# Kernel tuning notes

Measured on AMD Instinct MI355X. Metric: run time of the kernel, lower is better.

The kernel has to match this reference:

```python
import jax, jax.numpy as jnp
import numpy as np

N = 50000      # total packed nodes
E = 1600000    # edges (no self loops; layers add them)
G = 64         # graphs in the batch
F_IN = 24      # raw node feature dim
D = 64         # hidden dim
H = 4          # attention heads
C = D // H     # 16 channels per head
L = 3          # GAT layers
NEG = 0.2      # LeakyReLU negative slope (GATv2 default)
EPS = 1e-5     # LayerNorm eps


def setup_inputs() -> dict:
    key = jax.random.key(0)
    ks = jax.random.split(key, 16)
    x = jax.random.normal(ks[0], (N, F_IN), jnp.float32)
    src = jax.random.randint(ks[1], (E,), 0, N)
    dst = jax.random.randint(ks[2], (E,), 0, N)
    dst = jnp.where(dst == src, (dst + 1) % N, dst)  # keep edge list self-loop free
    edge_index = jnp.stack([src, dst]).astype(jnp.int32)
    batch = jnp.sort(jax.random.randint(ks[3], (N,), 0, G)).astype(jnp.int32)
    s = 0.1
    return dict(
        x=x, edge_index=edge_index, batch=batch,
        w_in=jax.random.normal(ks[4], (F_IN, D), jnp.float32) * s,
        b_in=jnp.zeros((D,), jnp.float32),
        w_l=jax.random.normal(ks[5], (L, D, D), jnp.float32) * s,
        b_l=jnp.zeros((L, D), jnp.float32),
        w_r=jax.random.normal(ks[6], (L, D, D), jnp.float32) * s,
        b_r=jnp.zeros((L, D), jnp.float32),
        att=jax.random.normal(ks[7], (L, H, C), jnp.float32) * s,
        b_gat=jnp.zeros((L, D), jnp.float32),
        ln_g=jnp.ones((L, D), jnp.float32),
        ln_b=jnp.zeros((L, D), jnp.float32),
        w_g1=jax.random.normal(ks[8], (D, D // 2), jnp.float32) * s,
        b_g1=jnp.zeros((D // 2,), jnp.float32),
        w_g2=jax.random.normal(ks[9], (D // 2, 1), jnp.float32) * s,
        b_g2=jnp.zeros((1,), jnp.float32),
        w_out=jax.random.normal(ks[10], (D, D), jnp.float32) * s,
        b_out=jnp.zeros((D,), jnp.float32),
    )


def _layernorm(h, g, b):
    m = h.mean(-1, keepdims=True)
    v = ((h - m) ** 2).mean(-1, keepdims=True)
    return (h - m) * jax.lax.rsqrt(v + EPS) * g + b


def _gatv2(h, src, dst, wl, bl, wr, br, att, bg):
    n = h.shape[0]
    xl = (h @ wl + bl).reshape(n, H, C)   # source transform
    xr = (h @ wr + br).reshape(n, H, C)   # target transform
    # edge scores: att . leaky_relu(xl[j] + xr[i])  -> [E', H]
    e = jnp.sum(jax.nn.leaky_relu(xl[src] + xr[dst], NEG) * att, axis=-1)
    emax = jax.ops.segment_max(e, dst, num_segments=n)
    ex = jnp.exp(e - emax[dst])
    denom = jax.ops.segment_sum(ex, dst, num_segments=n)
    alpha = ex / denom[dst]               # segment softmax over incoming edges
    out = jax.ops.segment_sum(alpha[:, :, None] * xl[src], dst, num_segments=n)
    return out.reshape(n, D) + bg


def reference(x, edge_index, batch, w_in, b_in, w_l, b_l, w_r, b_r, att, b_gat,
              ln_g, ln_b, w_g1, b_g1, w_g2, b_g2, w_out, b_out):
    n = x.shape[0]
    loops = jnp.arange(n, dtype=edge_index.dtype)
    src = jnp.concatenate([edge_index[0], loops])  # add self loops once
    dst = jnp.concatenate([edge_index[1], loops])
    h = jax.nn.relu(x @ w_in + b_in)
    for i in range(L):
        res = h
        h = _gatv2(h, src, dst, w_l[i], b_l[i], w_r[i], b_r[i], att[i], b_gat[i])
        h = _layernorm(h + res, ln_g[i], ln_b[i])
        if i < L - 1:
            h = jax.nn.relu(h)
    # GlobalAttention pooling: gate MLP -> per-graph softmax -> weighted sum
    gate = jax.nn.relu(h @ w_g1 + b_g1) @ w_g2 + b_g2  # [N, 1]
    gmax = jax.ops.segment_max(gate, batch, num_segments=G)
    ge = jnp.exp(gate - gmax[batch])
    gs = jax.ops.segment_sum(ge, batch, num_segments=G)
    a = ge / jnp.where(gs > 0, gs, 1.0)[batch]
    emb = jax.ops.segment_sum(a * h, batch, num_segments=G)  # [G, D]
    return jax.nn.relu(emb @ w_out + b_out)
```

## Files before the change

kernel.cpp:

```cpp
#include <hip/hip_runtime.h>

#define NEGS   0.2f
#define LN_EPS 1e-5f
#define BSH    7
#define BN     128
#define TILE   4096
#define LOG2E  1.44269504f

typedef const float* __restrict__ fp;
typedef _Float16 v2h __attribute__((ext_vector_type(2)));
typedef _Float16 v8h __attribute__((ext_vector_type(8)));
typedef float    v4f __attribute__((ext_vector_type(4)));

__device__ __forceinline__ v2h u2h(unsigned u){ union{unsigned u; v2h h;} c; c.u = u; return c.h; }
__device__ __forceinline__ unsigned h2u(v2h h){ union{v2h h; unsigned u;} c; c.h = h; return c.u; }

template<int CTRL>
__device__ __forceinline__ float dppadd(float x){
  int y = __builtin_amdgcn_update_dpp(0, __float_as_int(x), CTRL, 0xF, 0xF, true);
  return x + __int_as_float(y);
}
__device__ __forceinline__ float hsum8(float s){
  s = dppadd<0xB1>(s);
  s = dppadd<0x4E>(s);
  s = dppadd<0x141>(s);
  return s;
}

__device__ __forceinline__ float dot8(v8h a, v8h b, float init){
  union U { v8h v; v2h h[4]; };
  U ua; ua.v = a;
  U ub; ub.v = b;
  float s = init;
  #pragma unroll
  for (int i = 0; i < 4; ++i) s = __builtin_amdgcn_fdot2(ua.h[i], ub.h[i], s, false);
  return s;
}

__device__ __forceinline__ v8h leaky8(v8h t){
  return __builtin_elementwise_max(t, t * (_Float16)NEGS);
}

__device__ __forceinline__ float edge_w8(v8h v, v8h xr8, v8h att8, float negm2){
  v8h t = leaky8(v + xr8);
  float s = dppadd<0xB1>(dot8(t, att8, negm2));
  return __builtin_amdgcn_exp2f(s);
}

__global__ __launch_bounds__(256) void k_setup(fp x, fp w, fp b, float* __restrict__ h,
                                               unsigned* __restrict__ h16, int N,
                                               fp w_l, fp w_r, fp att,
                                               _Float16* __restrict__ wf, _Float16* __restrict__ att16,
                                               float* __restrict__ gz, int nz,
                                               const int* __restrict__ dstA, int* __restrict__ counts,
                                               int E, int K, int ntiles){
  __shared__ float ws[24*64];
  __shared__ float bs[64];
  __shared__ float xs[4][24];
  __shared__ int hist[512];
  int tid = threadIdx.x;
  if (blockIdx.x < 6){
    int lm = blockIdx.x;
    if (lm < 3){
      for (int d = tid; d < 64; d += 256)
        att16[lm*64 + d] = (_Float16)(att[lm*64 + d] * LOG2E);
    }
    for (int i = lm*256 + tid; i < nz; i += 6*256) gz[i] = 0.f;
    const float* src = ((lm & 1) ? w_r : w_l) + (lm >> 1)*4096;
    _Float16* dst = wf + lm*4096;
    for (int d = tid; d < 4096; d += 256){
      int jj = d & 7, l = (d >> 3) & 63, kc = (d >> 9) & 1, nt = d >> 10;
      int k = kc*32 + (l >> 4)*8 + jj;
      int n = nt*16 + (l & 15);
      dst[d] = (_Float16)src[k*64 + n];
    }
    return;
  }
  if (blockIdx.x < (unsigned)(6 + ntiles)){
    int t = blockIdx.x - 6;
    for (int i = tid; i < K; i += 256) hist[i] = 0;
    __syncthreads();
    int e0 = t*TILE, e1 = min(e0 + TILE, E);
    for (int e = e0 + tid; e < e1; e += 256)
      atomicAdd(&hist[dstA[e] >> BSH], 1);
    __syncthreads();
    for (int i = tid; i < K; i += 256) counts[i*ntiles + t] = hist[i];
    return;
  }
  int blk = blockIdx.x - 6 - ntiles;
  for (int i = tid; i < 24*64; i += 256) ws[i] = w[i];
  if (tid < 64) bs[tid] = b[tid];
  int r = tid >> 6, c = tid & 63;
  int row = blk*4 + r;
  if (c < 24 && row < N) xs[r][c] = x[row*24 + c];
  __syncthreads();
  float acc = bs[c];
  #pragma unroll
  for (int k = 0; k < 24; ++k) acc = fmaf(xs[r][k], ws[k*64 + c], acc);
  float y = fmaxf(acc, 0.f);
  float y1 = __shfl_down(y, 1);
  if (row < N){
    h[(size_t)row*64 + c] = y;
    if (!(c & 1)){
      v2h p; p.x = (_Float16)y; p.y = (_Float16)y1;
      h16[(size_t)row*32 + (c >> 1)] = h2u(p);
    }
  }
}

__global__ __launch_bounds__(512) void s_scan_tiles(int* __restrict__ counts, int* __restrict__ btotal,
                                                    int ntiles){
  __shared__ int s[512];
  int b = blockIdx.x, tid = threadIdx.x;
  int v = (tid < ntiles) ? counts[b*ntiles + tid] : 0;
  s[tid] = v;
  __syncthreads();
  for (int off = 1; off < 512; off <<= 1){
    int t = (tid >= off) ? s[tid - off] : 0;
    __syncthreads();
    s[tid] += t;
    __syncthreads();
  }
  if (tid < ntiles) counts[b*ntiles + tid] = s[tid] - v;
  if (tid == 511) btotal[b] = s[511];
}

__global__ __launch_bounds__(512) void s_scan_buckets(const int* __restrict__ btotal,
                                                      int* __restrict__ bbase, int K, int E){
  __shared__ int s[512];
  int tid = threadIdx.x;
  int v = (tid < K) ? btotal[tid] : 0;
  s[tid] = v;
  __syncthreads();
  for (int off = 1; off < 512; off <<= 1){
    int t = (tid >= off) ? s[tid - off] : 0;
    __syncthreads();
    s[tid] += t;
    __syncthreads();
  }
  if (tid < K) bbase[tid] = s[tid] - v;
  if (tid == 0) bbase[K] = E;
}

__global__ __launch_bounds__(256) void t_scatter(const int* __restrict__ srcA, const int* __restrict__ dstA,
                                                 const int* __restrict__ counts, const int* __restrict__ bbase,
                                                 unsigned* __restrict__ packed, int E, int K, int ntiles){
  __shared__ int gb[512];
  __shared__ int cur[512];
  int t = blockIdx.x, tid = threadIdx.x;
  for (int i = tid; i < K; i += 256){
    gb[i] = bbase[i] + counts[i*ntiles + t];
    cur[i] = 0;
  }
  __syncthreads();
  int e0 = t*TILE, e1 = min(e0 + TILE, E);
  for (int e = e0 + tid; e < e1; e += 256){
    int d = dstA[e], sv = srcA[e];
    int b = d >> BSH;
    int p = atomicAdd(&cur[b], 1);
    packed[gb[b] + p] = ((unsigned)(d & (BN-1)) << 25) | (unsigned)sv;
  }
}

__global__ __launch_bounds__(256) void k_finexfm(const unsigned* __restrict__ packed, const int* __restrict__ bbase,
                                                 int* __restrict__ row_ptr, int* __restrict__ col, int N, int K,
                                                 const unsigned* __restrict__ h16, const _Float16* __restrict__ wf,
                                                 fp blg, fp brg,
                                                 unsigned* __restrict__ xl16, unsigned* __restrict__ xr16){
  __shared__ int hist[BN];
  __shared__ int excl[BN];
  int tid = threadIdx.x;
  if (blockIdx.x < (unsigned)K){
    int b = blockIdx.x;
    int node0 = b << BSH;
    int e_base = bbase[b], e_end = bbase[b+1];
    if (tid < BN) hist[tid] = 0;
    __syncthreads();
    for (int e = e_base + tid; e < e_end; e += 256)
      atomicAdd(&hist[packed[e] >> 25], 1);
    __syncthreads();
    int v = (tid < BN) ? hist[tid] : 0;
    if (tid < BN) excl[tid] = v;
    __syncthreads();
    for (int off = 1; off < BN; off <<= 1){
      int t2 = 0;
      if (tid < BN && tid >= off) t2 = excl[tid - off];
      __syncthreads();
      if (tid < BN) excl[tid] += t2;
      __syncthreads();
    }
    int nn = min(BN, N - node0);
    if (tid < nn) row_ptr[node0 + tid] = e_base + excl[tid] - v;
    if (b == K-1 && tid == 0) row_ptr[N] = e_end;
    if (tid < BN) hist[tid] = excl[tid] - v;
    __syncthreads();
    for (int e = e_base + tid; e < e_end; e += 256){
      unsigned u = packed[e];
      int dl = u >> 25;
      int p = atomicAdd(&hist[dl], 1);
      col[e_base + p] = (int)(u & 0x1FFFFFFu);
    }
    return;
  }
  int xb = blockIdx.x - K;
  int wave = tid >> 6, lane = tid & 63;
  int quad = lane >> 4, ln = lane & 15;
  int m0 = xb*64 + wave*16;
  if (m0 >= N) return;
  int m = m0 + ln;
  bool mv = m < N;
  v8h a0 = {}, a1 = {};
  if (mv){
    a0 = *(const v8h*)&h16[(size_t)m*32 + quad*4];
    a1 = *(const v8h*)&h16[(size_t)m*32 + 16 + quad*4];
  }
  #pragma unroll
  for (int mat = 0; mat < 2; ++mat){
    const _Float16* wb = wf + mat*4096;
    fp bias = mat ? brg : blg;
    unsigned* dst = mat ? xr16 : xl16;
    #pragma unroll
    for (int nt = 0; nt < 4; ++nt){
      v8h b0 = *(const v8h*)&wb[nt*1024 + lane*8];
      v8h b1 = *(const v8h*)&wb[nt*1024 + 512 + lane*8];
      float bv = bias[nt*16 + ln];
      v4f acc = {bv, bv, bv, bv};
      acc = __builtin_amdgcn_mfma_f32_16x16x32_f16(a0, b0, acc, 0, 0, 0);
      acc = __builtin_amdgcn_mfma_f32_16x16x32_f16(a1, b1, acc, 0, 0, 0);
      #pragma unroll
      for (int r = 0; r < 4; ++r){
        float partner = __shfl_xor(acc[r], 1);
        int node = m0 + quad*4 + r;
        if (!(lane & 1) && node < N){
          v2h p; p.x = (_Float16)acc[r]; p.y = (_Float16)partner;
          dst[(size_t)node*32 + nt*8 + (ln >> 1)] = h2u(p);
        }
      }
    }
  }
}

__global__ __launch_bounds__(256) void k_xfm(const unsigned* __restrict__ h16,
                                             const _Float16* __restrict__ wf,
                                             fp blg, fp brg,
                                             unsigned* __restrict__ xl16, unsigned* __restrict__ xr16, int N){
  int tid = threadIdx.x, wave = tid >> 6, lane = tid & 63;
  int quad = lane >> 4, ln = lane & 15;
  int m0 = blockIdx.x*64 + wave*16;
  if (m0 >= N) return;
  int m = m0 + ln;
  bool mv = m < N;
  v8h a0 = {}, a1 = {};
  if (mv){
    a0 = *(const v8h*)&h16[(size_t)m*32 + quad*4];
    a1 = *(const v8h*)&h16[(size_t)m*32 + 16 + quad*4];
  }
  #pragma unroll
  for (int mat = 0; mat < 2; ++mat){
    const _Float16* wb = wf + mat*4096;
    fp bias = mat ? brg : blg;
    unsigned* dst = mat ? xr16 : xl16;
    #pragma unroll
    for (int nt = 0; nt < 4; ++nt){
      v8h b0 = *(const v8h*)&wb[nt*1024 + lane*8];
      v8h b1 = *(const v8h*)&wb[nt*1024 + 512 + lane*8];
      float bv = bias[nt*16 + ln];
      v4f acc = {bv, bv, bv, bv};
      acc = __builtin_amdgcn_mfma_f32_16x16x32_f16(a0, b0, acc, 0, 0, 0);
      acc = __builtin_amdgcn_mfma_f32_16x16x32_f16(a1, b1, acc, 0, 0, 0);
      #pragma unroll
      for (int r = 0; r < 4; ++r){
        float partner = __shfl_xor(acc[r], 1);
        int node = m0 + quad*4 + r;
        if (!(lane & 1) && node < N){
          v2h p; p.x = (_Float16)acc[r]; p.y = (_Float16)partner;
          dst[(size_t)node*32 + nt*8 + (ln >> 1)] = h2u(p);
        }
      }
    }
  }
}

__global__ __launch_bounds__(256) void k_gat(const unsigned* __restrict__ xl16, const unsigned* __restrict__ xr16,
                                             float* __restrict__ h, unsigned* __restrict__ h16,
                                             const int* __restrict__ row_ptr, const int* __restrict__ col,
                                             const _Float16* __restrict__ att16, fp bg, fp lng, fp lnb,
                                             int N, int do_relu){
  int lane = threadIdx.x & 63;
  int g = lane >> 3;
  int s = lane & 7;
  int node = (blockIdx.x*4 + (threadIdx.x >> 6))*8 + g;
  bool valid = node < N;
  int nodec = valid ? node : N - 1;

  v8h att8 = *(const v8h*)&att16[s*8];
  v8h xr8  = *(const v8h*)&xr16[(size_t)nodec*32 + s*4];
  v8h xl8  = *(const v8h*)&xl16[(size_t)nodec*32 + s*4];

  float m = dppadd<0xB1>(dot8(leaky8(xl8 + xr8), att8, 0.f));
  float negm2 = m * -0.5f;

  float den = 1.f;
  float acc[8];
  #pragma unroll
  for (int i = 0; i < 8; ++i) acc[i] = (float)xl8[i];

  int e  = row_ptr[nodec];
  int e1 = valid ? row_ptr[nodec + 1] : e;

  for (; e + 4 <= e1; e += 4){
    int j0 = col[e], j1 = col[e+1], j2 = col[e+2], j3 = col[e+3];
    v8h v0 = *(const v8h*)&xl16[(size_t)j0*32 + s*4];
    v8h v1 = *(const v8h*)&xl16[(size_t)j1*32 + s*4];
    v8h v2 = *(const v8h*)&xl16[(size_t)j2*32 + s*4];
    v8h v3 = *(const v8h*)&xl16[(size_t)j3*32 + s*4];
    float w0 = edge_w8(v0, xr8, att8, negm2);
    float w1 = edge_w8(v1, xr8, att8, negm2);
    float w2 = edge_w8(v2, xr8, att8, negm2);
    float w3 = edge_w8(v3, xr8, att8, negm2);
    den += (w0 + w1) + (w2 + w3);
    #pragma unroll
    for (int i = 0; i < 8; ++i){
      acc[i] = fmaf(w0, (float)v0[i], acc[i]);
      acc[i] = fmaf(w1, (float)v1[i], acc[i]);
      acc[i] = fmaf(w2, (float)v2[i], acc[i]);
      acc[i] = fmaf(w3, (float)v3[i], acc[i]);
    }
  }
  for (; e + 2 <= e1; e += 2){
    int j0 = col[e], j1 = col[e+1];
    v8h v0 = *(const v8h*)&xl16[(size_t)j0*32 + s*4];
    v8h v1 = *(const v8h*)&xl16[(size_t)j1*32 + s*4];
    float w0 = edge_w8(v0, xr8, att8, negm2);
    float w1 = edge_w8(v1, xr8, att8, negm2);
    den += w0 + w1;
    #pragma unroll
    for (int i = 0; i < 8; ++i){
      acc[i] = fmaf(w0, (float)v0[i], acc[i]);
      acc[i] = fmaf(w1, (float)v1[i], acc[i]);
    }
  }
  if (e < e1){
    int j0 = col[e];
    v8h v0 = *(const v8h*)&xl16[(size_t)j0*32 + s*4];
    float w0 = edge_w8(v0, xr8, att8, negm2);
    den += w0;
    #pragma unroll
    for (int i = 0; i < 8; ++i) acc[i] = fmaf(w0, (float)v0[i], acc[i]);
  }

  float inv = 1.f / den;

  float4 bgA = *(const float4*)&bg[s*8];
  float4 bgB = *(const float4*)&bg[s*8 + 4];
  float4 hA  = *(const float4*)&h[(size_t)nodec*64 + s*8];
  float4 hB  = *(const float4*)&h[(size_t)nodec*64 + s*8 + 4];
  float res8[8] = {hA.x + bgA.x, hA.y + bgA.y, hA.z + bgA.z, hA.w + bgA.w,
                   hB.x + bgB.x, hB.y + bgB.y, hB.z + bgB.z, hB.w + bgB.w};
  float o8[8];
  float sl = 0.f;
  #pragma unroll
  for (int i = 0; i < 8; ++i){ o8[i] = fmaf(acc[i], inv, res8[i]); sl += o8[i]; }
  sl = hsum8(sl);
  float mean = sl * (1.f/64.f);
  float vsl = 0.f;
  #pragma unroll
  for (int i = 0; i < 8; ++i){ o8[i] -= mean; vsl = fmaf(o8[i], o8[i], vsl); }
  vsl = hsum8(vsl);
  float rs = rsqrtf(vsl * (1.f/64.f) + LN_EPS);

  if (valid){
    float4 lgA = *(const float4*)&lng[s*8], lgB = *(const float4*)&lng[s*8 + 4];
    float4 lbA = *(const float4*)&lnb[s*8], lbB = *(const float4*)&lnb[s*8 + 4];
    float lg8[8] = {lgA.x, lgA.y, lgA.z, lgA.w, lgB.x, lgB.y, lgB.z, lgB.w};
    float lb8[8] = {lbA.x, lbA.y, lbA.z, lbA.w, lbB.x, lbB.y, lbB.z, lbB.w};
    float y[8];
    #pragma unroll
    for (int i = 0; i < 8; ++i){
      y[i] = fmaf(o8[i]*rs, lg8[i], lb8[i]);
      if (do_relu) y[i] = fmaxf(y[i], 0.f);
    }
    float4 yA = {y[0], y[1], y[2], y[3]};
    float4 yB = {y[4], y[5], y[6], y[7]};
    *(float4*)&h[(size_t)node*64 + s*8]     = yA;
    *(float4*)&h[(size_t)node*64 + s*8 + 4] = yB;
    v8h p;
    #pragma unroll
    for (int i = 0; i < 8; ++i) p[i] = (_Float16)y[i];
    *(v8h*)&h16[(size_t)node*32 + s*4] = p;
  }
}

__global__ __launch_bounds__(256) void k_gatemb(const float* __restrict__ h, fp w1, fp b1, fp w2, fp b2,
                                                const int* __restrict__ batch,
                                                float* __restrict__ gsum, float* __restrict__ embsum, int N){
  __shared__ float w1s[2048];
  __shared__ float hrow[16][64];
  __shared__ float sgate[16];
  __shared__ int sbatch[16];
  int tid = threadIdx.x;
  for (int i = tid*4; i < 2048; i += 1024) *(float4*)&w1s[i] = *(const float4*)&w1[i];
  int base = blockIdx.x*16;
  int nrows = min(16, N - base);
  int lim = nrows*64;
  for (int i = tid*4; i < lim; i += 1024)
    *(float4*)&hrow[0][i] = *(const float4*)&h[(size_t)base*64 + i];
  if (tid < nrows) sbatch[tid] = batch[base + tid];
  __syncthreads();
  int wave = tid >> 6, lane = tid & 63;
  int j = lane & 31, half = lane >> 5;
  float b1v = b1[j], w2v = w2[j], b2v = b2[0];
  int k0 = half*32;
  #pragma unroll
  for (int it = 0; it < 4; ++it){
    int r = wave*4 + it;
    if (base + r >= N) break;
    float s = 0.f;
    #pragma unroll 8
    for (int k = k0; k < k0 + 32; ++k) s = fmaf(hrow[r][k], w1s[k*32 + j], s);
    s += __shfl_xor(s, 32);
    float hid = fmaxf(s + b1v, 0.f);
    float contrib = (half == 0) ? hid * w2v : 0.f;
    #pragma unroll
    for (int o = 1; o < 64; o <<= 1) contrib += __shfl_xor(contrib, o);
    if (lane == 0) sgate[r] = contrib + b2v;
  }
  __syncthreads();
  if (wave == 0 && nrows > 0){
    int cur = sbatch[0];
    float acc = 0.f, asum = 0.f;
    for (int i = 0; i < nrows; ++i){
      int g = sbatch[i];
      if (g != cur){
        atomicAdd(&embsum[cur*64 + lane], acc);
        if (lane == 0) atomicAdd(&gsum[cur], asum);
        acc = 0.f; asum = 0.f; cur = g;
      }
      float a = __expf(sgate[i]);
      acc = fmaf(a, hrow[i][lane], acc);
      asum += a;
    }
    atomicAdd(&embsum[cur*64 + lane], acc);
    if (lane == 0) atomicAdd(&gsum[cur], asum);
  }
}

__global__ __launch_bounds__(64) void k_out(const float* __restrict__ embsum, const float* __restrict__ gsum,
                                            fp w_out, fp b_out, float* __restrict__ out, int G){
  int g = blockIdx.x, lane = threadIdx.x;
  __shared__ float emb[64];
  float gs = gsum[g];
  float inv = (gs > 0.f) ? 1.f/gs : 1.f;
  emb[lane] = embsum[g*64 + lane] * inv;
  __syncthreads();
  float o2 = b_out[lane];
  #pragma unroll 8
  for (int d = 0; d < 64; ++d) o2 = fmaf(emb[d], w_out[d*64 + lane], o2);
  out[g*64 + lane] = fmaxf(o2, 0.f);
}

extern "C" void kernel_launch(void* const* d_in, const int* in_sizes, int n_in,
                              void* d_out, int out_size, void* d_ws, size_t ws_size,
                              hipStream_t stream) {
  const int N = in_sizes[0] / 24;
  const int E = in_sizes[1] / 2;
  const int G = out_size / 64;
  const int K = (N + BN - 1) >> BSH;
  const int ntiles = (E + TILE - 1) / TILE;

  fp x      = (fp)d_in[0];
  const int* edge  = (const int*)d_in[1];
  const int* batch = (const int*)d_in[2];
  fp w_in   = (fp)d_in[3];
  fp b_in   = (fp)d_in[4];
  fp w_l    = (fp)d_in[5];
  fp b_l    = (fp)d_in[6];
  fp w_r    = (fp)d_in[7];
  fp b_r    = (fp)d_in[8];
  fp att    = (fp)d_in[9];
  fp b_gat  = (fp)d_in[10];
  fp ln_g   = (fp)d_in[11];
  fp ln_b   = (fp)d_in[12];
  fp w_g1   = (fp)d_in[13];
  fp b_g1   = (fp)d_in[14];
  fp w_g2   = (fp)d_in[15];
  fp b_g2   = (fp)d_in[16];
  fp w_out  = (fp)d_in[17];
  fp b_out  = (fp)d_in[18];
  float* out = (float*)d_out;

  char* wp = (char*)d_ws;
  auto alloc = [&](size_t bytes) -> char* {
    char* p = wp; wp += (bytes + 255) & ~(size_t)255; return p;
  };
  float*    h       = (float*)    alloc((size_t)N*64*sizeof(float));
  unsigned* h16     = (unsigned*) alloc((size_t)N*32*sizeof(unsigned));
  unsigned* xl16    = (unsigned*) alloc((size_t)N*32*sizeof(unsigned));
  unsigned* xr16    = (unsigned*) alloc((size_t)N*32*sizeof(unsigned));
  int*      col     = (int*)      alloc((size_t)E*sizeof(int));
  unsigned* packed  = (unsigned*) alloc((size_t)E*sizeof(unsigned));
  int*      counts  = (int*)      alloc((size_t)K*ntiles*sizeof(int));
  int*      btotal  = (int*)      alloc((size_t)K*sizeof(int));
  int*      bbase   = (int*)      alloc((size_t)(K+1)*sizeof(int));
  int*      row_ptr = (int*)      alloc((size_t)(N+1)*sizeof(int));
  float*    gsum    = (float*)    alloc((size_t)(G + G*64)*sizeof(float));
  float*    embsum  = gsum + G;
  _Float16* wf      = (_Float16*) alloc((size_t)3*2*4096*sizeof(_Float16));
  _Float16* att16g  = (_Float16*) alloc((size_t)3*64*sizeof(_Float16));

  const int* srcA = edge;
  const int* dstA = edge + E;

  k_setup<<<6 + ntiles + (N + 3)/4, 256, 0, stream>>>(x, w_in, b_in, h, h16, N, w_l, w_r, att,
                                                      wf, att16g, gsum, G + G*64,
                                                      dstA, counts, E, K, ntiles);

  s_scan_tiles<<<K, 512, 0, stream>>>(counts, btotal, ntiles);
  s_scan_buckets<<<1, 512, 0, stream>>>(btotal, bbase, K, E);
  t_scatter<<<ntiles, 256, 0, stream>>>(srcA, dstA, counts, bbase, packed, E, K, ntiles);

  k_finexfm<<<K + (N + 63)/64, 256, 0, stream>>>(packed, bbase, row_ptr, col, N, K,
                                                 h16, wf, b_l, b_r, xl16, xr16);

  for (int i = 0; i < 3; ++i){
    if (i > 0)
      k_xfm<<<(N + 63)/64, 256, 0, stream>>>(h16, wf + i*8192, b_l + i*64, b_r + i*64,
                                             xl16, xr16, N);
    k_gat<<<(N + 31)/32, 256, 0, stream>>>(xl16, xr16, h, h16, row_ptr, col,
                                           att16g + i*64, b_gat + i*64, ln_g + i*64, ln_b + i*64,
                                           N, i < 2 ? 1 : 0);
  }

  k_gatemb<<<(N + 15)/16, 256, 0, stream>>>(h, w_g1, b_g1, w_g2, b_g2, batch, gsum, embsum, N);
  k_out<<<G, 64, 0, stream>>>(embsum, gsum, w_out, b_out, out, G);
}
```

Before: 310.5 us.

## Fuse scan and output kernels via last-block tickets; unroll edge loop to 8

```diff
diff --git a/kernel.cpp b/kernel.cpp
--- a/kernel.cpp
+++ b/kernel.cpp
@@ -51,7 +51,7 @@
                                                unsigned* __restrict__ h16, int N,
                                                fp w_l, fp w_r, fp att,
                                                _Float16* __restrict__ wf, _Float16* __restrict__ att16,
-                                               float* __restrict__ gz, int nz,
+                                               float* __restrict__ gz, int nz, int* __restrict__ ticket,
                                                const int* __restrict__ dstA, int* __restrict__ counts,
                                                int E, int K, int ntiles){
   __shared__ float ws[24*64];
@@ -61,6 +61,7 @@
   int tid = threadIdx.x;
   if (blockIdx.x < 6){
     int lm = blockIdx.x;
+    if (lm == 0 && tid == 0){ ticket[0] = 0; ticket[1] = 0; }
     if (lm < 3){
       for (int d = tid; d < 64; d += 256)
         att16[lm*64 + d] = (_Float16)(att[lm*64 + d] * LOG2E);
@@ -108,9 +109,11 @@
   }
 }
 
-__global__ __launch_bounds__(512) void s_scan_tiles(int* __restrict__ counts, int* __restrict__ btotal,
-                                                    int ntiles){
+__global__ __launch_bounds__(512) void s_scan(int* __restrict__ counts, int* __restrict__ btotal,
+                                              int* __restrict__ bbase, int* __restrict__ ticket,
+                                              int ntiles, int K, int E){
   __shared__ int s[512];
+  __shared__ int lastf;
   int b = blockIdx.x, tid = threadIdx.x;
   int v = (tid < ntiles) ? counts[b*ntiles + tid] : 0;
   s[tid] = v;
@@ -122,15 +125,17 @@
     __syncthreads();
   }
   if (tid < ntiles) counts[b*ntiles + tid] = s[tid] - v;
-  if (tid == 511) btotal[b] = s[511];
-}
-
-__global__ __launch_bounds__(512) void s_scan_buckets(const int* __restrict__ btotal,
-                                                      int* __restrict__ bbase, int K, int E){
-  __shared__ int s[512];
-  int tid = threadIdx.x;
-  int v = (tid < K) ? btotal[tid] : 0;
-  s[tid] = v;
+  if (tid == 511) atomicExch(&btotal[b], s[511]);
+  __syncthreads();
+  if (tid == 0){
+    __threadfence();
+    lastf = (atomicAdd(ticket, 1) == (int)gridDim.x - 1);
+  }
+  __syncthreads();
+  if (!lastf) return;
+  __threadfence();
+  int v2 = (tid < K) ? atomicAdd(&btotal[tid], 0) : 0;
+  s[tid] = v2;
   __syncthreads();
   for (int off = 1; off < 512; off <<= 1){
     int t = (tid >= off) ? s[tid - off] : 0;
@@ -138,7 +143,7 @@
     s[tid] += t;
     __syncthreads();
   }
-  if (tid < K) bbase[tid] = s[tid] - v;
+  if (tid < K) bbase[tid] = s[tid] - v2;
   if (tid == 0) bbase[K] = E;
 }
 
@@ -308,23 +313,38 @@
   int e  = row_ptr[nodec];
   int e1 = valid ? row_ptr[nodec + 1] : e;
 
-  for (; e + 4 <= e1; e += 4){
-    int j0 = col[e], j1 = col[e+1], j2 = col[e+2], j3 = col[e+3];
+  for (; e + 8 <= e1; e += 8){
+    int j0 = col[e],   j1 = col[e+1], j2 = col[e+2], j3 = col[e+3];
+    int j4 = col[e+4], j5 = col[e+5], j6 = col[e+6], j7 = col[e+7];
     v8h v0 = *(const v8h*)&xl16[(size_t)j0*32 + s*4];
     v8h v1 = *(const v8h*)&xl16[(size_t)j1*32 + s*4];
     v8h v2 = *(const v8h*)&xl16[(size_t)j2*32 + s*4];
     v8h v3 = *(const v8h*)&xl16[(size_t)j3*32 + s*4];
+    v8h v4 = *(const v8h*)&xl16[(size_t)j4*32 + s*4];
+    v8h v5 = *(const v8h*)&xl16[(size_t)j5*32 + s*4];
+    v8h v6 = *(const v8h*)&xl16[(size_t)j6*32 + s*4];
+    v8h v7 = *(const v8h*)&xl16[(size_t)j7*32 + s*4];
     float w0 = edge_w8(v0, xr8, att8, negm2);
     float w1 = edge_w8(v1, xr8, att8, negm2);
     float w2 = edge_w8(v2, xr8, att8, negm2);
     float w3 = edge_w8(v3, xr8, att8, negm2);
-    den += (w0 + w1) + (w2 + w3);
+    float w4 = edge_w8(v4, xr8, att8, negm2);
+    float w5 = edge_w8(v5, xr8, att8, negm2);
+    float w6 = edge_w8(v6, xr8, att8, negm2);
+    float w7 = edge_w8(v7, xr8, att8, negm2);
+    den += ((w0 + w1) + (w2 + w3)) + ((w4 + w5) + (w6 + w7));
     #pragma unroll
     for (int i = 0; i < 8; ++i){
-      acc[i] = fmaf(w0, (float)v0[i], acc[i]);
-      acc[i] = fmaf(w1, (float)v1[i], acc[i]);
-      acc[i] = fmaf(w2, (float)v2[i], acc[i]);
-      acc[i] = fmaf(w3, (float)v3[i], acc[i]);
+      float a = acc[i];
+      a = fmaf(w0, (float)v0[i], a);
+      a = fmaf(w1, (float)v1[i], a);
+      a = fmaf(w2, (float)v2[i], a);
+      a = fmaf(w3, (float)v3[i], a);
+      a = fmaf(w4, (float)v4[i], a);
+      a = fmaf(w5, (float)v5[i], a);
+      a = fmaf(w6, (float)v6[i], a);
+      a = fmaf(w7, (float)v7[i], a);
+      acc[i] = a;
     }
   }
   for (; e + 2 <= e1; e += 2){
@@ -392,12 +412,16 @@
 }
 
 __global__ __launch_bounds__(256) void k_gatemb(const float* __restrict__ h, fp w1, fp b1, fp w2, fp b2,
-                                                const int* __restrict__ batch,
-                                                float* __restrict__ gsum, float* __restrict__ embsum, int N){
+                                                const int* __restrict__ batch, fp w_out, fp b_out,
+                                                float* __restrict__ gsum, float* __restrict__ embsum,
+                                                float* __restrict__ out, int* __restrict__ ticket,
+                                                int N, int G){
   __shared__ float w1s[2048];
   __shared__ float hrow[16][64];
   __shared__ float sgate[16];
   __shared__ int sbatch[16];
+  __shared__ float sembs[4][64];
+  __shared__ int lastf;
   int tid = threadIdx.x;
   for (int i = tid*4; i < 2048; i += 1024) *(float4*)&w1s[i] = *(const float4*)&w1[i];
   int base = blockIdx.x*16;
@@ -443,20 +467,23 @@
     atomicAdd(&embsum[cur*64 + lane], acc);
     if (lane == 0) atomicAdd(&gsum[cur], asum);
   }
-}
-
-__global__ __launch_bounds__(64) void k_out(const float* __restrict__ embsum, const float* __restrict__ gsum,
-                                            fp w_out, fp b_out, float* __restrict__ out, int G){
-  int g = blockIdx.x, lane = threadIdx.x;
-  __shared__ float emb[64];
-  float gs = gsum[g];
-  float inv = (gs > 0.f) ? 1.f/gs : 1.f;
-  emb[lane] = embsum[g*64 + lane] * inv;
-  __syncthreads();
-  float o2 = b_out[lane];
-  #pragma unroll 8
-  for (int d = 0; d < 64; ++d) o2 = fmaf(emb[d], w_out[d*64 + lane], o2);
-  out[g*64 + lane] = fmaxf(o2, 0.f);
+  __syncthreads();
+  if (tid == 0){
+    __threadfence();
+    lastf = (atomicAdd(ticket, 1) == (int)gridDim.x - 1);
+  }
+  __syncthreads();
+  if (!lastf) return;
+  __threadfence();
+  for (int g0 = wave; g0 < G; g0 += 4){
+    float gs = atomicAdd(&gsum[g0], 0.f);
+    float inv = (gs > 0.f) ? 1.f/gs : 1.f;
+    sembs[wave][lane] = atomicAdd(&embsum[g0*64 + lane], 0.f) * inv;
+    float o2 = b_out[lane];
+    #pragma unroll 8
+    for (int d = 0; d < 64; ++d) o2 = fmaf(sembs[wave][d], w_out[d*64 + lane], o2);
+    out[g0*64 + lane] = fmaxf(o2, 0.f);
+  }
 }
 
 extern "C" void kernel_launch(void* const* d_in, const int* in_sizes, int n_in,
@@ -507,16 +534,16 @@
   float*    embsum  = gsum + G;
   _Float16* wf      = (_Float16*) alloc((size_t)3*2*4096*sizeof(_Float16));
   _Float16* att16g  = (_Float16*) alloc((size_t)3*64*sizeof(_Float16));
+  int*      ticket  = (int*)      alloc(2*sizeof(int));
 
   const int* srcA = edge;
   const int* dstA = edge + E;
 
   k_setup<<<6 + ntiles + (N + 3)/4, 256, 0, stream>>>(x, w_in, b_in, h, h16, N, w_l, w_r, att,
-                                                      wf, att16g, gsum, G + G*64,
+                                                      wf, att16g, gsum, G + G*64, ticket,
                                                       dstA, counts, E, K, ntiles);
 
-  s_scan_tiles<<<K, 512, 0, stream>>>(counts, btotal, ntiles);
-  s_scan_buckets<<<1, 512, 0, stream>>>(btotal, bbase, K, E);
+  s_scan<<<K, 512, 0, stream>>>(counts, btotal, bbase, ticket + 0, ntiles, K, E);
   t_scatter<<<ntiles, 256, 0, stream>>>(srcA, dstA, counts, bbase, packed, E, K, ntiles);
 
   k_finexfm<<<K + (N + 63)/64, 256, 0, stream>>>(packed, bbase, row_ptr, col, N, K,
@@ -531,6 +558,6 @@
                                            N, i < 2 ? 1 : 0);
   }
 
-  k_gatemb<<<(N + 15)/16, 256, 0, stream>>>(h, w_g1, b_g1, w_g2, b_g2, batch, gsum, embsum, N);
-  k_out<<<G, 64, 0, stream>>>(embsum, gsum, w_out, b_out, out, G);
-}
+  k_gatemb<<<(N + 15)/16, 256, 0, stream>>>(h, w_g1, b_g1, w_g2, b_g2, batch, w_out, b_out,
+                                            gsum, embsum, out, ticket + 1, N, G);
+}
```

Measured after the change: 452.9 us. +45.9%, slower.

## Replace bucketed two-pass CSR build with global-atomic degree count and scatter

Applied to the files above, without the earlier changes.

```diff
diff --git a/kernel.cpp b/kernel.cpp
--- a/kernel.cpp
+++ b/kernel.cpp
@@ -2,8 +2,6 @@
 
 #define NEGS   0.2f
 #define LN_EPS 1e-5f
-#define BSH    7
-#define BN     128
 #define TILE   4096
 #define LOG2E  1.44269504f
 
@@ -51,13 +49,11 @@
                                                unsigned* __restrict__ h16, int N,
                                                fp w_l, fp w_r, fp att,
                                                _Float16* __restrict__ wf, _Float16* __restrict__ att16,
-                                               float* __restrict__ gz, int nz,
-                                               const int* __restrict__ dstA, int* __restrict__ counts,
-                                               int E, int K, int ntiles){
+                                               const int* __restrict__ dstA, int* __restrict__ deg,
+                                               int E, int ntiles){
   __shared__ float ws[24*64];
   __shared__ float bs[64];
   __shared__ float xs[4][24];
-  __shared__ int hist[512];
   int tid = threadIdx.x;
   if (blockIdx.x < 6){
     int lm = blockIdx.x;
@@ -65,7 +61,6 @@
       for (int d = tid; d < 64; d += 256)
         att16[lm*64 + d] = (_Float16)(att[lm*64 + d] * LOG2E);
     }
-    for (int i = lm*256 + tid; i < nz; i += 6*256) gz[i] = 0.f;
     const float* src = ((lm & 1) ? w_r : w_l) + (lm >> 1)*4096;
     _Float16* dst = wf + lm*4096;
     for (int d = tid; d < 4096; d += 256){
@@ -78,13 +73,9 @@
   }
   if (blockIdx.x < (unsigned)(6 + ntiles)){
     int t = blockIdx.x - 6;
-    for (int i = tid; i < K; i += 256) hist[i] = 0;
-    __syncthreads();
     int e0 = t*TILE, e1 = min(e0 + TILE, E);
     for (int e = e0 + tid; e < e1; e += 256)
-      atomicAdd(&hist[dstA[e] >> BSH], 1);
-    __syncthreads();
-    for (int i = tid; i < K; i += 256) counts[i*ntiles + t] = hist[i];
+      atomicAdd(&deg[dstA[e]], 1);
     return;
   }
   int blk = blockIdx.x - 6 - ntiles;
@@ -108,101 +99,50 @@
   }
 }
 
-__global__ __launch_bounds__(512) void s_scan_tiles(int* __restrict__ counts, int* __restrict__ btotal,
-                                                    int ntiles){
-  __shared__ int s[512];
-  int b = blockIdx.x, tid = threadIdx.x;
-  int v = (tid < ntiles) ? counts[b*ntiles + tid] : 0;
-  s[tid] = v;
+__global__ __launch_bounds__(1024) void s_scan_nodes(const int* __restrict__ deg,
+                                                     int* __restrict__ row_ptr, int* __restrict__ wcur,
+                                                     int N, int E){
+  __shared__ int ssum[1024];
+  int tid = threadIdx.x;
+  int per = (N + 1023) >> 10;
+  int start = tid * per, end = min(start + per, N);
+  int s = 0;
+  for (int i = start; i < end; ++i) s += deg[i];
+  ssum[tid] = s;
   __syncthreads();
-  for (int off = 1; off < 512; off <<= 1){
-    int t = (tid >= off) ? s[tid - off] : 0;
+  for (int off = 1; off < 1024; off <<= 1){
+    int t = (tid >= off) ? ssum[tid - off] : 0;
     __syncthreads();
-    s[tid] += t;
+    ssum[tid] += t;
     __syncthreads();
   }
-  if (tid < ntiles) counts[b*ntiles + tid] = s[tid] - v;
-  if (tid == 511) btotal[b] = s[511];
-}
-
-__global__ __launch_bounds__(512) void s_scan_buckets(const int* __restrict__ btotal,
-                                                      int* __restrict__ bbase, int K, int E){
-  __shared__ int s[512];
-  int tid = threadIdx.x;
-  int v = (tid < K) ? btotal[tid] : 0;
-  s[tid] = v;
-  __syncthreads();
-  for (int off = 1; off < 512; off <<= 1){
-    int t = (tid >= off) ? s[tid - off] : 0;
-    __syncthreads();
-    s[tid] += t;
-    __syncthreads();
-  }
-  if (tid < K) bbase[tid] = s[tid] - v;
-  if (tid == 0) bbase[K] = E;
-}
-
-__global__ __launch_bounds__(256) void t_scatter(const int* __restrict__ srcA, const int* __restrict__ dstA,
-                                                 const int* __restrict__ counts, const int* __restrict__ bbase,
-                                                 unsigned* __restrict__ packed, int E, int K, int ntiles){
-  __shared__ int gb[512];
-  __shared__ int cur[512];
-  int t = blockIdx.x, tid = threadIdx.x;
-  for (int i = tid; i < K; i += 256){
-    gb[i] = bbase[i] + counts[i*ntiles + t];
-    cur[i] = 0;
-  }
-  __syncthreads();
-  int e0 = t*TILE, e1 = min(e0 + TILE, E);
-  for (int e = e0 + tid; e < e1; e += 256){
-    int d = dstA[e], sv = srcA[e];
-    int b = d >> BSH;
-    int p = atomicAdd(&cur[b], 1);
-    packed[gb[b] + p] = ((unsigned)(d & (BN-1)) << 25) | (unsigned)sv;
-  }
-}
-
-__global__ __launch_bounds__(256) void k_finexfm(const unsigned* __restrict__ packed, const int* __restrict__ bbase,
-                                                 int* __restrict__ row_ptr, int* __restrict__ col, int N, int K,
+  int run = (tid == 0) ? 0 : ssum[tid - 1];
+  for (int i = start; i < end; ++i){
+    row_ptr[i] = run;
+    wcur[i] = run;
+    run += deg[i];
+  }
+  if (tid == 0) row_ptr[N] = E;
+}
+
+__global__ __launch_bounds__(256) void k_scatxfm(const int* __restrict__ srcA, const int* __restrict__ dstA,
+                                                 int* __restrict__ wcur, int* __restrict__ col,
+                                                 int E, int ntiles,
                                                  const unsigned* __restrict__ h16, const _Float16* __restrict__ wf,
                                                  fp blg, fp brg,
-                                                 unsigned* __restrict__ xl16, unsigned* __restrict__ xr16){
-  __shared__ int hist[BN];
-  __shared__ int excl[BN];
+                                                 unsigned* __restrict__ xl16, unsigned* __restrict__ xr16, int N){
   int tid = threadIdx.x;
-  if (blockIdx.x < (unsigned)K){
-    int b = blockIdx.x;
-    int node0 = b << BSH;
-    int e_base = bbase[b], e_end = bbase[b+1];
-    if (tid < BN) hist[tid] = 0;
-    __syncthreads();
-    for (int e = e_base + tid; e < e_end; e += 256)
-      atomicAdd(&hist[packed[e] >> 25], 1);
-    __syncthreads();
-    int v = (tid < BN) ? hist[tid] : 0;
-    if (tid < BN) excl[tid] = v;
-    __syncthreads();
-    for (int off = 1; off < BN; off <<= 1){
-      int t2 = 0;
-      if (tid < BN && tid >= off) t2 = excl[tid - off];
-      __syncthreads();
-      if (tid < BN) excl[tid] += t2;
-      __syncthreads();
-    }
-    int nn = min(BN, N - node0);
-    if (tid < nn) row_ptr[node0 + tid] = e_base + excl[tid] - v;
-    if (b == K-1 && tid == 0) row_ptr[N] = e_end;
-    if (tid < BN) hist[tid] = excl[tid] - v;
-    __syncthreads();
-    for (int e = e_base + tid; e < e_end; e += 256){
-      unsigned u = packed[e];
-      int dl = u >> 25;
-      int p = atomicAdd(&hist[dl], 1);
-      col[e_base + p] = (int)(u & 0x1FFFFFFu);
+  if (blockIdx.x < (unsigned)ntiles){
+    int t = blockIdx.x;
+    int e0 = t*TILE, e1 = min(e0 + TILE, E);
+    for (int e = e0 + tid; e < e1; e += 256){
+      int d = dstA[e];
+      int pos = atomicAdd(&wcur[d], 1);
+      col[pos] = srcA[e];
     }
     return;
   }
-  int xb = blockIdx.x - K;
+  int xb = blockIdx.x - ntiles;
   int wave = tid >> 6, lane = tid & 63;
   int quad = lane >> 4, ln = lane & 15;
   int m0 = xb*64 + wave*16;
@@ -465,7 +405,6 @@
   const int N = in_sizes[0] / 24;
   const int E = in_sizes[1] / 2;
   const int G = out_size / 64;
-  const int K = (N + BN - 1) >> BSH;
   const int ntiles = (E + TILE - 1) / TILE;
 
   fp x      = (fp)d_in[0];
@@ -498,11 +437,9 @@
   unsigned* xl16    = (unsigned*) alloc((size_t)N*32*sizeof(unsigned));
   unsigned* xr16    = (unsigned*) alloc((size_t)N*32*sizeof(unsigned));
   int*      col     = (int*)      alloc((size_t)E*sizeof(int));
-  unsigned* packed  = (unsigned*) alloc((size_t)E*sizeof(unsigned));
-  int*      counts  = (int*)      alloc((size_t)K*ntiles*sizeof(int));
-  int*      btotal  = (int*)      alloc((size_t)K*sizeof(int));
-  int*      bbase   = (int*)      alloc((size_t)(K+1)*sizeof(int));
   int*      row_ptr = (int*)      alloc((size_t)(N+1)*sizeof(int));
+  int*      wcur    = (int*)      alloc((size_t)N*sizeof(int));
+  int*      deg     = (int*)      alloc((size_t)N*sizeof(int));
   float*    gsum    = (float*)    alloc((size_t)(G + G*64)*sizeof(float));
   float*    embsum  = gsum + G;
   _Float16* wf      = (_Float16*) alloc((size_t)3*2*4096*sizeof(_Float16));
@@ -511,16 +448,16 @@
   const int* srcA = edge;
   const int* dstA = edge + E;
 
+  size_t zbytes = (size_t)((char*)(gsum + G + G*64) - (char*)deg);
+  hipMemsetAsync(deg, 0, zbytes, stream);
+
   k_setup<<<6 + ntiles + (N + 3)/4, 256, 0, stream>>>(x, w_in, b_in, h, h16, N, w_l, w_r, att,
-                                                      wf, att16g, gsum, G + G*64,
-                                                      dstA, counts, E, K, ntiles);
-
-  s_scan_tiles<<<K, 512, 0, stream>>>(counts, btotal, ntiles);
-  s_scan_buckets<<<1, 512, 0, stream>>>(btotal, bbase, K, E);
-  t_scatter<<<ntiles, 256, 0, stream>>>(srcA, dstA, counts, bbase, packed, E, K, ntiles);
-
-  k_finexfm<<<K + (N + 63)/64, 256, 0, stream>>>(packed, bbase, row_ptr, col, N, K,
-                                                 h16, wf, b_l, b_r, xl16, xr16);
+                                                      wf, att16g, dstA, deg, E, ntiles);
+
+  s_scan_nodes<<<1, 1024, 0, stream>>>(deg, row_ptr, wcur, N, E);
+
+  k_scatxfm<<<ntiles + (N + 63)/64, 256, 0, stream>>>(srcA, dstA, wcur, col, E, ntiles,
+                                                      h16, wf, b_l, b_r, xl16, xr16, N);
 
   for (int i = 0; i < 3; ++i){
     if (i > 0)
```

New measurement: 588.1 us. 1.89x slower.

## Fold bucket and tile prefix scans into the scatter kernel

Applied to the files above, without the earlier changes.

```diff
diff --git a/kernel.cpp b/kernel.cpp
--- a/kernel.cpp
+++ b/kernel.cpp
@@ -108,53 +108,40 @@
   }
 }
 
-__global__ __launch_bounds__(512) void s_scan_tiles(int* __restrict__ counts, int* __restrict__ btotal,
-                                                    int ntiles){
-  __shared__ int s[512];
-  int b = blockIdx.x, tid = threadIdx.x;
-  int v = (tid < ntiles) ? counts[b*ntiles + tid] : 0;
-  s[tid] = v;
-  __syncthreads();
-  for (int off = 1; off < 512; off <<= 1){
-    int t = (tid >= off) ? s[tid - off] : 0;
-    __syncthreads();
-    s[tid] += t;
-    __syncthreads();
-  }
-  if (tid < ntiles) counts[b*ntiles + tid] = s[tid] - v;
-  if (tid == 511) btotal[b] = s[511];
-}
-
-__global__ __launch_bounds__(512) void s_scan_buckets(const int* __restrict__ btotal,
-                                                      int* __restrict__ bbase, int K, int E){
-  __shared__ int s[512];
-  int tid = threadIdx.x;
-  int v = (tid < K) ? btotal[tid] : 0;
-  s[tid] = v;
-  __syncthreads();
-  for (int off = 1; off < 512; off <<= 1){
-    int t = (tid >= off) ? s[tid - off] : 0;
-    __syncthreads();
-    s[tid] += t;
-    __syncthreads();
-  }
-  if (tid < K) bbase[tid] = s[tid] - v;
-  if (tid == 0) bbase[K] = E;
-}
-
-__global__ __launch_bounds__(256) void t_scatter(const int* __restrict__ srcA, const int* __restrict__ dstA,
-                                                 const int* __restrict__ counts, const int* __restrict__ bbase,
-                                                 unsigned* __restrict__ packed, int E, int K, int ntiles){
+__global__ __launch_bounds__(512) void t_scatter2(const int* __restrict__ srcA, const int* __restrict__ dstA,
+                                                  const int* __restrict__ counts, int* __restrict__ bbase,
+                                                  unsigned* __restrict__ packed, int E, int K, int ntiles){
+  __shared__ int sS[512];
   __shared__ int gb[512];
   __shared__ int cur[512];
   int t = blockIdx.x, tid = threadIdx.x;
-  for (int i = tid; i < K; i += 256){
-    gb[i] = bbase[i] + counts[i*ntiles + t];
-    cur[i] = 0;
-  }
+  int S = 0, P = 0;
+  if (tid < K){
+    const int* row = counts + (size_t)tid*ntiles;
+    for (int j = 0; j < ntiles; ++j){
+      int c = row[j];
+      S += c;
+      P += (j < t) ? c : 0;
+    }
+  }
+  sS[tid] = S;
+  __syncthreads();
+  for (int off = 1; off < 512; off <<= 1){
+    int v = (tid >= off) ? sS[tid - off] : 0;
+    __syncthreads();
+    sS[tid] += v;
+    __syncthreads();
+  }
+  if (tid < K){
+    int B = sS[tid] - S;
+    gb[tid] = B + P;
+    cur[tid] = 0;
+    if (t == 0) bbase[tid] = B;
+  }
+  if (t == 0 && tid == 0) bbase[K] = E;
   __syncthreads();
   int e0 = t*TILE, e1 = min(e0 + TILE, E);
-  for (int e = e0 + tid; e < e1; e += 256){
+  for (int e = e0 + tid; e < e1; e += 512){
     int d = dstA[e], sv = srcA[e];
     int b = d >> BSH;
     int p = atomicAdd(&cur[b], 1);
@@ -500,7 +487,6 @@
   int*      col     = (int*)      alloc((size_t)E*sizeof(int));
   unsigned* packed  = (unsigned*) alloc((size_t)E*sizeof(unsigned));
   int*      counts  = (int*)      alloc((size_t)K*ntiles*sizeof(int));
-  int*      btotal  = (int*)      alloc((size_t)K*sizeof(int));
   int*      bbase   = (int*)      alloc((size_t)(K+1)*sizeof(int));
   int*      row_ptr = (int*)      alloc((size_t)(N+1)*sizeof(int));
   float*    gsum    = (float*)    alloc((size_t)(G + G*64)*sizeof(float));
@@ -515,9 +501,7 @@
                                                       wf, att16g, gsum, G + G*64,
                                                       dstA, counts, E, K, ntiles);
 
-  s_scan_tiles<<<K, 512, 0, stream>>>(counts, btotal, ntiles);
-  s_scan_buckets<<<1, 512, 0, stream>>>(btotal, bbase, K, E);
-  t_scatter<<<ntiles, 256, 0, stream>>>(srcA, dstA, counts, bbase, packed, E, K, ntiles);
+  t_scatter2<<<ntiles, 512, 0, stream>>>(srcA, dstA, counts, bbase, packed, E, K, ntiles);
 
   k_finexfm<<<K + (N + 63)/64, 256, 0, stream>>>(packed, bbase, row_ptr, col, N, K,
                                                  h16, wf, b_l, b_r, xl16, xr16);
```

Measured after the change: 418.4 us. 34.8% more time.
